# Kernel optimization log

Measured on AMD Instinct MI355X. Metric: run time of the kernel, lower is better.

## Reference

```python
import jax, jax.numpy as jnp
import numpy as np

B, N_SPINS, D_MODEL, K_MC = 256, 128, 768, 25


def setup_inputs() -> dict:
    key = jax.random.key(0)
    k1, k2, k3 = jax.random.split(key, 3)
    features = jax.random.normal(k1, (B, N_SPINS, D_MODEL), dtype=jnp.float32)
    coalitions = jax.random.randint(k2, (K_MC, N_SPINS), 0, 2, dtype=jnp.int32)
    w_v = jax.random.normal(k3, (D_MODEL, D_MODEL), dtype=jnp.float32) * 0.02
    scale = jnp.full((1,), 0.1, dtype=jnp.float32)
    return {"features": features, "coalitions": coalitions, "w_v": w_v, "scale": scale}


def reference(features, coalitions, w_v, scale):
    # features: [B, n, d]; coalitions: [K, n] in {0,1}; w_v: [d, d]; scale: [1]
    c = coalitions.astype(features.dtype)                      # [K, n]
    # coalition_value batched over all K coalitions at once:
    # sum_j mask[k,j] * features[b,j,:]  (sum and linear proj commute)
    s = jnp.einsum('kn,bnd->bkd', c, features)                 # [B, K, d]
    proj = s @ w_v                                             # [B, K, d]
    norm = jnp.linalg.norm(proj, axis=-1)                      # [B, K]
    cv = jax.nn.relu(norm * scale[0])                          # coalition values [B, K]
    # Shapley estimate: mean(v | i in S) - mean(v | i not in S)
    cnt_with = c.sum(axis=0)                                   # [n]
    cnt_without = c.shape[0] - cnt_with
    v_with = (cv @ c) / jnp.maximum(cnt_with, 1.0)             # [B, n]
    v_without = (cv @ (1.0 - c)) / jnp.maximum(cnt_without, 1.0)
    valid = (cnt_with > 0) & (cnt_without > 0)                 # [n]
    shapley = jnp.where(valid, v_with - v_without, 0.0)        # [B, n]
    return shapley
```

## Files before the change

kernel.cpp:

```cpp
#include <hip/hip_runtime.h>
#include <hip/hip_bf16.h>
#include <stdint.h>

#define NB  256
#define NSP 128
#define DM  768
#define KMC 25
#define MROWS (NB*KMC)

#define OFF_S    0u
#define OFF_WT   9830400u
#define OFF_N2   11010048u
#define OFF_COEF 11035648u
#define OFF_CB   11049984u

typedef __attribute__((ext_vector_type(8))) short bf16x8;
typedef __attribute__((ext_vector_type(4))) float f32x4;
typedef unsigned int u32;

#define GLOAD_LDS16(gp, lp) \
  __builtin_amdgcn_global_load_lds((const __attribute__((address_space(1))) u32*)(gp), \
                                   (__attribute__((address_space(3))) u32*)(lp), 16, 0, 0)

__global__ __launch_bounds__(256) void prep_kernel(const float* __restrict__ wv,
                                                   const int* __restrict__ co,
                                                   char* __restrict__ ws) {
  const int blk = blockIdx.x;
  const int t = threadIdx.x;
  if (blk < 144) {
    __shared__ __hip_bfloat16 lt[64][66];
    const int bi = blk / 12, bj = blk % 12;
    const int k0 = bi * 64, n0 = bj * 64;
    #pragma unroll
    for (int i = 0; i < 16; ++i) {
      int idx = t + i * 256;
      int r = idx >> 6, c = idx & 63;
      lt[c][r] = __float2bfloat16(wv[(size_t)(k0 + r) * DM + n0 + c]);
    }
    __syncthreads();
    __hip_bfloat16* wT = (__hip_bfloat16*)(ws + OFF_WT);
    #pragma unroll
    for (int i = 0; i < 16; ++i) {
      int idx = t + i * 256;
      int r = idx >> 6, c = idx & 63;
      wT[(size_t)(n0 + r) * DM + k0 + c] = lt[r][c];
    }
  } else if (blk == 144) {
    if (t < NSP) {
      const int n = t;
      int cw = 0;
      #pragma unroll
      for (int k = 0; k < KMC; ++k) cw += co[k * NSP + n];
      const int cwo = KMC - cw;
      const bool valid = (cw > 0) && (cwo > 0);
      float* coefT = (float*)(ws + OFF_COEF);
      #pragma unroll
      for (int k = 0; k < 28; ++k) {
        float v = 0.f;
        if (valid && k < KMC) v = co[k * NSP + n] ? (1.f / (float)cw) : (-1.f / (float)cwo);
        coefT[n * 28 + k] = v;
      }
    }
  } else if (blk < 170) {
    int i = (blk - 145) * 256 + t;
    if (i < MROWS) ((float*)(ws + OFF_N2))[i] = 0.f;
  } else {
    int k = blk - 170;
    if (t < NSP) {
      float v = (k < KMC) ? (float)co[k * NSP + t] : 0.f;
      ((__hip_bfloat16*)(ws + OFF_CB))[k * NSP + t] = __float2bfloat16(v);
    }
  }
}

#define KBPW 196

__global__ __launch_bounds__(256, 4) void kA(const float* __restrict__ f,
                                             const __hip_bfloat16* __restrict__ Cb,
                                             __hip_bfloat16* __restrict__ s) {
  const int b = blockIdx.x;
  const int slice = blockIdx.y;
  const int tid = threadIdx.x;
  const int w = tid >> 6;
  const int lane = tid & 63;
  const int lo = lane & 15, hi = lane >> 4;

  __shared__ __align__(16) unsigned short Fs[2][32 * KBPW];

  bf16x8 A0[4], A1[4];
  #pragma unroll
  for (int ks = 0; ks < 4; ++ks) {
    A0[ks] = *(const bf16x8*)(Cb + (size_t)lo * NSP + ks * 32 + hi * 8);
    A1[ks] = *(const bf16x8*)(Cb + (size_t)(16 + lo) * NSP + ks * 32 + hi * 8);
  }

  int goff[6], waddr[6];
  #pragma unroll
  for (int p = 0; p < 6; ++p) {
    int e = 4 * tid + 1024 * p;
    int r = e / 192, c = e - r * 192;
    goff[p] = r * DM + c;
    waddr[p] = r * KBPW + c;
  }

  const float* fb = f + (size_t)b * NSP * DM + slice * 192;

  f32x4 ac0[3], ac1[3];
  #pragma unroll
  for (int ct = 0; ct < 3; ++ct)
    #pragma unroll
    for (int i = 0; i < 4; ++i) { ac0[ct][i] = 0.f; ac1[ct][i] = 0.f; }

  float4 rA[6];

#define KA_LOAD(ck) { \
    const float* fp_ = fb + (size_t)(ck) * 32 * DM; \
    _Pragma("unroll") for (int p = 0; p < 6; ++p) \
      rA[p] = *(const float4*)(fp_ + goff[p]); }

#define KA_STORE(bi) { \
    _Pragma("unroll") for (int p = 0; p < 6; ++p) { \
      __hip_bfloat16 h0_ = __float2bfloat16(rA[p].x); \
      __hip_bfloat16 h1_ = __float2bfloat16(rA[p].y); \
      __hip_bfloat16 h2_ = __float2bfloat16(rA[p].z); \
      __hip_bfloat16 h3_ = __float2bfloat16(rA[p].w); \
      u32 w0_ = (u32)*(unsigned short*)&h0_ | ((u32)*(unsigned short*)&h1_ << 16); \
      u32 w1_ = (u32)*(unsigned short*)&h2_ | ((u32)*(unsigned short*)&h3_ << 16); \
      u32* d_ = (u32*)&Fs[bi][waddr[p]]; \
      d_[0] = w0_; d_[1] = w1_; } }

#define KA_MFMA(ck, bi) { \
    _Pragma("unroll") for (int ct = 0; ct < 3; ++ct) { \
      bf16x8 Bf; \
      _Pragma("unroll") for (int j = 0; j < 8; ++j) \
        Bf[j] = (short)Fs[bi][(hi * 8 + j) * KBPW + w * 48 + ct * 16 + lo]; \
      ac0[ct] = __builtin_amdgcn_mfma_f32_16x16x32_bf16(A0[ck], Bf, ac0[ct], 0, 0, 0); \
      ac1[ct] = __builtin_amdgcn_mfma_f32_16x16x32_bf16(A1[ck], Bf, ac1[ct], 0, 0, 0); } }

  KA_LOAD(0)
  KA_STORE(0)
  __syncthreads();
  KA_LOAD(1)
  KA_MFMA(0, 0)
  KA_STORE(1)
  __syncthreads();
  KA_LOAD(2)
  KA_MFMA(1, 1)
  KA_STORE(0)
  __syncthreads();
  KA_LOAD(3)
  KA_MFMA(2, 0)
  KA_STORE(1)
  __syncthreads();
  KA_MFMA(3, 1)

#undef KA_LOAD
#undef KA_STORE
#undef KA_MFMA

  #pragma unroll
  for (int ct = 0; ct < 3; ++ct) {
    int dcol = slice * 192 + w * 48 + ct * 16 + lo;
    #pragma unroll
    for (int i = 0; i < 4; ++i) {
      int r0 = hi * 4 + i;
      s[((size_t)b * KMC + r0) * DM + dcol] = __float2bfloat16(ac0[ct][i]);
      int r1 = 16 + hi * 4 + i;
      if (r1 < KMC)
        s[((size_t)b * KMC + r1) * DM + dcol] = __float2bfloat16(ac1[ct][i]);
    }
  }
}

#define BM 128
#define BN 192
#define BK 32
#define NTK 24

__global__ __launch_bounds__(256) void kB(char* __restrict__ ws) {
  const int bid = blockIdx.x;
  const int tm = bid >> 2;
  const int tn = bid & 3;
  const int tid = threadIdx.x;
  const int wid = tid >> 6;
  const int lane = tid & 63;
  const int wm = wid >> 1;
  const int wn = wid & 1;

  const __hip_bfloat16* S  = (const __hip_bfloat16*)(ws + OFF_S);
  const __hip_bfloat16* WT = (const __hip_bfloat16*)(ws + OFF_WT);
  float* norm2 = (float*)(ws + OFF_N2);

  __shared__ __align__(16) char As[2][BM * BK * 2];
  __shared__ __align__(16) char Bs[2][BN * BK * 2];

  const char* gA[2]; char *lA0[2], *lA1[2];
  #pragma unroll
  for (int j = 0; j < 2; ++j) {
    int li = (wid * 2 + j) * 64 + lane;
    int r = li >> 2, sl = li & 3;
    int slx = sl ^ ((r >> 1) & 3);
    gA[j] = (const char*)(S + (size_t)(tm * BM + r) * DM) + slx * 16;
    lA0[j] = As[0] + (wid * 2 + j) * 1024;
    lA1[j] = As[1] + (wid * 2 + j) * 1024;
  }
  const char* gB[3]; char *lB0[3], *lB1[3];
  #pragma unroll
  for (int j = 0; j < 3; ++j) {
    int li = (wid * 3 + j) * 64 + lane;
    int r = li >> 2, sl = li & 3;
    int slx = sl ^ ((r >> 1) & 3);
    gB[j] = (const char*)(WT + (size_t)(tn * BN + r) * DM) + slx * 16;
    lB0[j] = Bs[0] + (wid * 3 + j) * 1024;
    lB1[j] = Bs[1] + (wid * 3 + j) * 1024;
  }

  auto stage = [&](int tk, int bsel) {
    size_t koff = (size_t)tk * (BK * 2);
    #pragma unroll
    for (int j = 0; j < 2; ++j) GLOAD_LDS16(gA[j] + koff, bsel ? lA1[j] : lA0[j]);
    #pragma unroll
    for (int j = 0; j < 3; ++j) GLOAD_LDS16(gB[j] + koff, bsel ? lB1[j] : lB0[j]);
  };

  f32x4 acc[4][6];
  #pragma unroll
  for (int m = 0; m < 4; ++m)
    #pragma unroll
    for (int n = 0; n < 6; ++n)
      #pragma unroll
      for (int j = 0; j < 4; ++j) acc[m][n][j] = 0.f;

  int offA[4], offB[6];
  #pragma unroll
  for (int m = 0; m < 4; ++m) {
    int r = wm * 64 + m * 16 + (lane & 15);
    int sl = (lane >> 4) ^ ((r >> 1) & 3);
    offA[m] = r * 64 + sl * 16;
  }
  #pragma unroll
  for (int n = 0; n < 6; ++n) {
    int r = wn * 96 + n * 16 + (lane & 15);
    int sl = (lane >> 4) ^ ((r >> 1) & 3);
    offB[n] = r * 64 + sl * 16;
  }

  stage(0, 0);
  for (int tk = 0; tk < NTK; ++tk) {
    int cur = tk & 1;
    __syncthreads();
    if (tk + 1 < NTK) stage(tk + 1, cur ^ 1);
    bf16x8 af[4], bfr[6];
    #pragma unroll
    for (int m = 0; m < 4; ++m) af[m] = *(const bf16x8*)(As[cur] + offA[m]);
    #pragma unroll
    for (int n = 0; n < 6; ++n) bfr[n] = *(const bf16x8*)(Bs[cur] + offB[n]);
    #pragma unroll
    for (int m = 0; m < 4; ++m)
      #pragma unroll
      for (int n = 0; n < 6; ++n)
        acc[m][n] = __builtin_amdgcn_mfma_f32_16x16x32_bf16(af[m], bfr[n], acc[m][n], 0, 0, 0);
  }

  float ps[4][4];
  #pragma unroll
  for (int m = 0; m < 4; ++m)
    #pragma unroll
    for (int i = 0; i < 4; ++i) {
      float v = 0.f;
      #pragma unroll
      for (int n = 0; n < 6; ++n) { float x = acc[m][n][i]; v += x * x; }
      #pragma unroll
      for (int d = 1; d < 16; d <<= 1) v += __shfl_xor(v, d, 64);
      ps[m][i] = v;
    }
  if ((lane & 15) == 0) {
    int g = lane >> 4;
    #pragma unroll
    for (int m = 0; m < 4; ++m)
      #pragma unroll
      for (int i = 0; i < 4; ++i)
        atomicAdd(&norm2[tm * BM + wm * 64 + m * 16 + g * 4 + i], ps[m][i]);
  }
}

__global__ __launch_bounds__(128) void kC(const char* __restrict__ ws,
                                          const float* __restrict__ scale,
                                          float* __restrict__ out) {
  const int b = blockIdx.x, n = threadIdx.x;
  const float* norm2 = (const float*)(ws + OFF_N2);
  const float* coefT = (const float*)(ws + OFF_COEF);
  __shared__ float cvs[32];
  if (n < KMC) {
    float nv = norm2[b * KMC + n];
    cvs[n] = fmaxf(sqrtf(fmaxf(nv, 0.f)) * scale[0], 0.f);
  } else if (n < 32) {
    cvs[n] = 0.f;
  }
  __syncthreads();
  float sum = 0.f;
  #pragma unroll
  for (int k = 0; k < KMC; ++k) sum += cvs[k] * coefT[n * 28 + k];
  out[b * NSP + n] = sum;
}

extern "C" void kernel_launch(void* const* d_in, const int* in_sizes, int n_in,
                              void* d_out, int out_size, void* d_ws, size_t ws_size,
                              hipStream_t stream) {
  const float* features   = (const float*)d_in[0];
  const int*   coalitions = (const int*)d_in[1];
  const float* wv         = (const float*)d_in[2];
  const float* scale      = (const float*)d_in[3];
  char* ws = (char*)d_ws;

  prep_kernel<<<202, 256, 0, stream>>>(wv, coalitions, ws);
  dim3 gaa(NB, 4);
  kA<<<gaa, 256, 0, stream>>>(features, (const __hip_bfloat16*)(ws + OFF_CB),
                              (__hip_bfloat16*)(ws + OFF_S));
  kB<<<200, 256, 0, stream>>>(ws);
  kC<<<NB, 128, 0, stream>>>(ws, scale, (float*)d_out);
}
```

Before: 49.62 us.

## Stream fp32 features into LDS via async global_load_lds with triple buffering

The kA feature loads now use direct global-to-LDS async copies (global_load_lds) of fp32 data instead of loading through registers and converting to bf16 before the LDS store. A triple-buffered LDS ring with explicit vmcnt waits and barriers keeps three chunks in flight. Conversion to bf16 moves to the LDS read path just before the MFMA. This removes VGPR staging and lets more memory traffic overlap compute. The cost is doubled LDS footprint (fp32, three buffers), occupancy lowered to 2 blocks per SM, and possible bank conflicts on the strided fp32 reads.

```diff
diff --git a/kernel.cpp b/kernel.cpp
--- a/kernel.cpp
+++ b/kernel.cpp
@@ -21,6 +21,9 @@
 #define GLOAD_LDS16(gp, lp) \
   __builtin_amdgcn_global_load_lds((const __attribute__((address_space(1))) u32*)(gp), \
                                    (__attribute__((address_space(3))) u32*)(lp), 16, 0, 0)
+
+#define KA_WAITV_BAR(N) asm volatile("s_waitcnt vmcnt(" #N ")\n\ts_barrier" ::: "memory")
+#define KA_BAR()        asm volatile("s_waitcnt lgkmcnt(0)\n\ts_barrier" ::: "memory")
 
 __global__ __launch_bounds__(256) void prep_kernel(const float* __restrict__ wv,
                                                    const int* __restrict__ co,
@@ -73,9 +76,7 @@
   }
 }
 
-#define KBPW 196
-
-__global__ __launch_bounds__(256, 4) void kA(const float* __restrict__ f,
+__global__ __launch_bounds__(256, 2) void kA(const float* __restrict__ f,
                                              const __hip_bfloat16* __restrict__ Cb,
                                              __hip_bfloat16* __restrict__ s) {
   const int b = blockIdx.x;
@@ -85,7 +86,7 @@
   const int lane = tid & 63;
   const int lo = lane & 15, hi = lane >> 4;
 
-  __shared__ __align__(16) unsigned short Fs[2][32 * KBPW];
+  __shared__ __align__(16) float Fs[3][32 * 192];
 
   bf16x8 A0[4], A1[4];
   #pragma unroll
@@ -94,13 +95,12 @@
     A1[ks] = *(const bf16x8*)(Cb + (size_t)(16 + lo) * NSP + ks * 32 + hi * 8);
   }
 
-  int goff[6], waddr[6];
-  #pragma unroll
-  for (int p = 0; p < 6; ++p) {
-    int e = 4 * tid + 1024 * p;
+  int goff[6];
+  #pragma unroll
+  for (int q = 0; q < 6; ++q) {
+    int e = (w * 6 + q) * 256 + lane * 4;
     int r = e / 192, c = e - r * 192;
-    goff[p] = r * DM + c;
-    waddr[p] = r * KBPW + c;
+    goff[q] = r * DM + c;
   }
 
   const float* fb = f + (size_t)b * NSP * DM + slice * 192;
@@ -111,51 +111,36 @@
     #pragma unroll
     for (int i = 0; i < 4; ++i) { ac0[ct][i] = 0.f; ac1[ct][i] = 0.f; }
 
-  float4 rA[6];
-
-#define KA_LOAD(ck) { \
+#define KA_ISSUE(ck, bi) { \
     const float* fp_ = fb + (size_t)(ck) * 32 * DM; \
-    _Pragma("unroll") for (int p = 0; p < 6; ++p) \
-      rA[p] = *(const float4*)(fp_ + goff[p]); }
-
-#define KA_STORE(bi) { \
-    _Pragma("unroll") for (int p = 0; p < 6; ++p) { \
-      __hip_bfloat16 h0_ = __float2bfloat16(rA[p].x); \
-      __hip_bfloat16 h1_ = __float2bfloat16(rA[p].y); \
-      __hip_bfloat16 h2_ = __float2bfloat16(rA[p].z); \
-      __hip_bfloat16 h3_ = __float2bfloat16(rA[p].w); \
-      u32 w0_ = (u32)*(unsigned short*)&h0_ | ((u32)*(unsigned short*)&h1_ << 16); \
-      u32 w1_ = (u32)*(unsigned short*)&h2_ | ((u32)*(unsigned short*)&h3_ << 16); \
-      u32* d_ = (u32*)&Fs[bi][waddr[p]]; \
-      d_[0] = w0_; d_[1] = w1_; } }
+    _Pragma("unroll") for (int q = 0; q < 6; ++q) \
+      GLOAD_LDS16(fp_ + goff[q], (char*)&Fs[(bi)][0] + ((w * 6 + q) << 10)); }
 
 #define KA_MFMA(ck, bi) { \
     _Pragma("unroll") for (int ct = 0; ct < 3; ++ct) { \
       bf16x8 Bf; \
-      _Pragma("unroll") for (int j = 0; j < 8; ++j) \
-        Bf[j] = (short)Fs[bi][(hi * 8 + j) * KBPW + w * 48 + ct * 16 + lo]; \
+      _Pragma("unroll") for (int j = 0; j < 8; ++j) { \
+        float v_ = Fs[(bi)][(hi * 8 + j) * 192 + w * 48 + ct * 16 + lo]; \
+        __hip_bfloat16 h_ = __float2bfloat16(v_); \
+        Bf[j] = *(short*)&h_; } \
       ac0[ct] = __builtin_amdgcn_mfma_f32_16x16x32_bf16(A0[ck], Bf, ac0[ct], 0, 0, 0); \
       ac1[ct] = __builtin_amdgcn_mfma_f32_16x16x32_bf16(A1[ck], Bf, ac1[ct], 0, 0, 0); } }
 
-  KA_LOAD(0)
-  KA_STORE(0)
-  __syncthreads();
-  KA_LOAD(1)
+  KA_ISSUE(0, 0)
+  KA_ISSUE(1, 1)
+  KA_ISSUE(2, 2)
+  KA_WAITV_BAR(12);
   KA_MFMA(0, 0)
-  KA_STORE(1)
-  __syncthreads();
-  KA_LOAD(2)
+  KA_BAR();
+  KA_ISSUE(3, 0)
+  KA_WAITV_BAR(12);
   KA_MFMA(1, 1)
-  KA_STORE(0)
-  __syncthreads();
-  KA_LOAD(3)
-  KA_MFMA(2, 0)
-  KA_STORE(1)
-  __syncthreads();
-  KA_MFMA(3, 1)
-
-#undef KA_LOAD
-#undef KA_STORE
+  KA_WAITV_BAR(6);
+  KA_MFMA(2, 2)
+  KA_WAITV_BAR(0);
+  KA_MFMA(3, 0)
+
+#undef KA_ISSUE
 #undef KA_MFMA
 
   #pragma unroll
```

After: 50.36 us. No clear change (+1.5%).
